# Kernel tuning notes

Hardware: AMD Instinct MI355X
Metric: run time of the kernel (lower is better)

The kernel has to match this reference:

```python
import jax, jax.numpy as jnp
import numpy as np

N = 2048
H = 128
W = 128
NEAR = 0.1


def _quat_to_rotmat(q):
    # q: [N,4] (w,x,y,z), normalized -> [N,3,3]
    q = q / jnp.clip(jnp.linalg.norm(q, axis=1, keepdims=True), 1e-8)
    w, x, y, z = q[:, 0], q[:, 1], q[:, 2], q[:, 3]
    xx, yy, zz = x * x, y * y, z * z
    xy, xz, yz = x * y, x * z, y * z
    wx, wy, wz = w * x, w * y, w * z
    r0 = jnp.stack([1 - 2 * (yy + zz), 2 * (xy - wz), 2 * (xz + wy)], axis=1)
    r1 = jnp.stack([2 * (xy + wz), 1 - 2 * (xx + zz), 2 * (yz - wx)], axis=1)
    r2 = jnp.stack([2 * (xz - wy), 2 * (yz + wx), 1 - 2 * (xx + yy)], axis=1)
    return jnp.stack([r0, r1, r2], axis=1)


def _covariance_matrices(log_scales, rotations):
    # R diag(s^2) R^T + 1e-6 I, per Gaussian
    s2 = jnp.exp(2.0 * log_scales)  # scales**2
    R = _quat_to_rotmat(rotations)  # [N,3,3]
    cov = jnp.einsum('nij,nj,nkj->nik', R, s2, R)
    return cov + 1e-6 * jnp.eye(3, dtype=cov.dtype)


def _render(means, cov3d, colors, opacities, intrinsics, camera_to_world, height, width):
    dt = means.dtype
    Rcw = camera_to_world[:3, :3]
    tcw = camera_to_world[:3, 3]
    Rwc = Rcw.T
    twc = -Rwc @ tcw
    p = means @ Rwc.T + twc  # [N,3] camera-space
    x, y, z = p[:, 0], p[:, 1], p[:, 2]
    valid = (z > NEAR).astype(dt)
    zc = jnp.maximum(z, NEAR)
    fx, fy = intrinsics[0, 0], intrinsics[1, 1]
    cx, cy = intrinsics[0, 2], intrinsics[1, 2]
    u = fx * x / zc + cx
    v = fy * y / zc + cy
    # EWA projection Jacobian [N,2,3]
    zeros = jnp.zeros_like(zc)
    J0 = jnp.stack([fx / zc, zeros, -fx * x / (zc * zc)], axis=1)
    J1 = jnp.stack([zeros, fy / zc, -fy * y / (zc * zc)], axis=1)
    J = jnp.stack([J0, J1], axis=1)
    cov_cam = jnp.einsum('ij,njk,lk->nil', Rwc, cov3d, Rwc)  # [N,3,3]
    cov2d = jnp.einsum('nij,njk,nlk->nil', J, cov_cam, J) + 0.3 * jnp.eye(2, dtype=dt)
    a, b, c = cov2d[:, 0, 0], cov2d[:, 0, 1], cov2d[:, 1, 1]
    det = jnp.maximum(a * c - b * b, 1e-12)
    cA, cB, cC = c / det, -b / det, a / det  # conic (inverse 2D covariance)
    # front-to-back depth order; invalid Gaussians pushed to the back
    order = jnp.argsort(jnp.where(valid > 0, zc, jnp.inf))
    u, v = u[order], v[order]
    cA, cB, cC = cA[order], cB[order], cC[order]
    op = (opacities * valid)[order]
    cols = colors[order]
    xs = jnp.arange(width, dtype=dt)
    ys = jnp.arange(height, dtype=dt)
    dx = xs[None, None, :] - u[:, None, None]  # [N,1,W] -> broadcasts
    dy = ys[None, :, None] - v[:, None, None]  # [N,H,1]
    power = (-0.5 * (cA[:, None, None] * dx * dx + cC[:, None, None] * dy * dy)
             - cB[:, None, None] * dx * dy)  # [N,H,W]
    power = jnp.minimum(power, 0.0)
    alpha = jnp.clip(op[:, None, None] * jnp.exp(power), 0.0, 0.99)
    Tcum = jnp.cumprod(1.0 - alpha, axis=0)
    Texcl = jnp.concatenate([jnp.ones_like(Tcum[:1]), Tcum[:-1]], axis=0)
    weight = alpha * Texcl  # [N,H,W]
    img = jnp.einsum('nhw,nc->hwc', weight, cols)  # [H,W,3]
    return img


def setup_inputs():
    key = jax.random.key(0)
    k = jax.random.split(key, 6)
    xy = jax.random.uniform(k[0], (N, 2), minval=-2.0, maxval=2.0)
    z = jax.random.uniform(k[1], (N, 1), minval=3.0, maxval=9.0)
    means = jnp.concatenate([xy, z], axis=1)
    log_scales = jnp.log(jax.random.uniform(k[2], (N, 3), minval=0.02, maxval=0.2))
    rotations = jax.random.normal(k[3], (N, 4))
    colors = jax.random.uniform(k[4], (N, 3))
    opacities = jax.random.normal(k[5], (N,))
    intrinsics = jnp.array([[150.0, 0.0, W / 2], [0.0, 150.0, H / 2], [0.0, 0.0, 1.0]], dtype=jnp.float32)
    camera_to_world = jnp.eye(4, dtype=jnp.float32)
    return {"means": means, "log_scales": log_scales, "rotations": rotations,
            "colors": colors, "opacities": opacities, "intrinsics": intrinsics,
            "camera_to_world": camera_to_world, "height": H, "width": W}


def reference(means, log_scales, rotations, colors, opacities, intrinsics, camera_to_world, height, width):
    cov3d = _covariance_matrices(log_scales, rotations)
    return _render(means, cov3d, jnp.clip(colors, 0.0, 1.0), jax.nn.sigmoid(opacities),
                   intrinsics, camera_to_world, height, width)
```

## Files before the change

### kernel.cpp

```cpp
#include <hip/hip_runtime.h>
#include <hip/hip_bf16.h>

#define NMAX 2048
#define HH 128
#define WW 128
#define NSEG 8
#define SEG 256
#define NEARP 0.1f

static __device__ __forceinline__ float ldin(const void* p, int i, bool is32) {
    return is32 ? ((const float*)p)[i]
                : __bfloat162float(((const __hip_bfloat16*)p)[i]);
}
static __device__ __forceinline__ bool detect32(const void* intr) {
    return ((const float*)intr)[0] > 1.0f;
}
static __device__ __forceinline__ void stout(void* out, int i, float v, bool is32) {
    if (is32) ((float*)out)[i] = v;
    else      ((__hip_bfloat16*)out)[i] = __float2bfloat16(v);
}


__global__ __launch_bounds__(256) void gs_preprocess(
    const void* __restrict__ means,
    const void* __restrict__ log_scales,
    const void* __restrict__ rots,
    const void* __restrict__ colors,
    const void* __restrict__ opac,
    const void* __restrict__ intr,
    const void* __restrict__ c2w,
    int n,
    unsigned long long* __restrict__ keys,
    float* __restrict__ params)
{
    int i = blockIdx.x * blockDim.x + threadIdx.x;
    if (i >= NMAX) return;
    bool is32 = detect32(intr);
    if (i >= n) {
        keys[i] = (((unsigned long long)0x7f800000u) << 32) | (unsigned int)i;
        return;
    }

    float Rwc[3][3], twc[3];
    {
        float Rcw[3][3], tcw[3];
        for (int r = 0; r < 3; ++r) {
            for (int c = 0; c < 3; ++c) Rcw[r][c] = ldin(c2w, r * 4 + c, is32);
            tcw[r] = ldin(c2w, r * 4 + 3, is32);
        }
        for (int r = 0; r < 3; ++r)
            for (int c = 0; c < 3; ++c) Rwc[r][c] = Rcw[c][r];
        for (int r = 0; r < 3; ++r)
            twc[r] = -(Rwc[r][0] * tcw[0] + Rwc[r][1] * tcw[1] + Rwc[r][2] * tcw[2]);
    }
    float fx = ldin(intr, 0, is32), fy = ldin(intr, 4, is32);
    float cx = ldin(intr, 2, is32), cy = ldin(intr, 5, is32);

    float mx = ldin(means, 3 * i, is32), my = ldin(means, 3 * i + 1, is32),
          mz = ldin(means, 3 * i + 2, is32);
    float px = Rwc[0][0] * mx + Rwc[0][1] * my + Rwc[0][2] * mz + twc[0];
    float py = Rwc[1][0] * mx + Rwc[1][1] * my + Rwc[1][2] * mz + twc[1];
    float pz = Rwc[2][0] * mx + Rwc[2][1] * my + Rwc[2][2] * mz + twc[2];
    bool valid = pz > NEARP;
    float zc = fmaxf(pz, NEARP);
    float izc = 1.0f / zc;
    float u = fx * px * izc + cx;
    float v = fy * py * izc + cy;

    float qw = ldin(rots, 4 * i, is32), qx = ldin(rots, 4 * i + 1, is32),
          qy = ldin(rots, 4 * i + 2, is32), qz = ldin(rots, 4 * i + 3, is32);
    float nrm = sqrtf(qw * qw + qx * qx + qy * qy + qz * qz);
    float inv = 1.0f / fmaxf(nrm, 1e-8f);
    qw *= inv; qx *= inv; qy *= inv; qz *= inv;
    float xx = qx * qx, yy = qy * qy, zz = qz * qz;
    float xy = qx * qy, xz = qx * qz, yz = qy * qz;
    float wx = qw * qx, wy = qw * qy, wz = qw * qz;
    float R[3][3] = {
        {1.f - 2.f * (yy + zz), 2.f * (xy - wz),       2.f * (xz + wy)},
        {2.f * (xy + wz),       1.f - 2.f * (xx + zz), 2.f * (yz - wx)},
        {2.f * (xz - wy),       2.f * (yz + wx),       1.f - 2.f * (xx + yy)}
    };
    float s2[3];
    for (int k = 0; k < 3; ++k) s2[k] = __expf(2.0f * ldin(log_scales, 3 * i + k, is32));

    float M[3][3];
    for (int r = 0; r < 3; ++r)
        for (int c = 0; c < 3; ++c)
            M[r][c] = R[r][0] * s2[0] * R[c][0] + R[r][1] * s2[1] * R[c][1]
                    + R[r][2] * s2[2] * R[c][2];
    M[0][0] += 1e-6f; M[1][1] += 1e-6f; M[2][2] += 1e-6f;

    float TM[3][3];
    for (int r = 0; r < 3; ++r)
        for (int c = 0; c < 3; ++c)
            TM[r][c] = Rwc[r][0] * M[0][c] + Rwc[r][1] * M[1][c] + Rwc[r][2] * M[2][c];
    float CC[3][3];
    for (int r = 0; r < 3; ++r)
        for (int c = 0; c < 3; ++c)
            CC[r][c] = TM[r][0] * Rwc[c][0] + TM[r][1] * Rwc[c][1] + TM[r][2] * Rwc[c][2];

    float J0[3] = {fx * izc, 0.0f, -fx * px * izc * izc};
    float J1[3] = {0.0f, fy * izc, -fy * py * izc * izc};
    float t0[3], t1[3];
    for (int c = 0; c < 3; ++c) {
        t0[c] = J0[0] * CC[0][c] + J0[1] * CC[1][c] + J0[2] * CC[2][c];
        t1[c] = J1[0] * CC[0][c] + J1[1] * CC[1][c] + J1[2] * CC[2][c];
    }
    float a  = t0[0] * J0[0] + t0[1] * J0[1] + t0[2] * J0[2] + 0.3f;
    float bq = t0[0] * J1[0] + t0[1] * J1[1] + t0[2] * J1[2];
    float cq = t1[0] * J1[0] + t1[1] * J1[1] + t1[2] * J1[2] + 0.3f;
    float det = fmaxf(a * cq - bq * bq, 1e-12f);
    float idet = 1.0f / det;
    float cA = cq * idet, cB = -bq * idet, cCc = a * idet;

    float o  = ldin(opac, i, is32);
    float op = valid ? (1.0f / (1.0f + __expf(-o))) : 0.0f;
    float cr = fminf(fmaxf(ldin(colors, 3 * i, is32), 0.f), 1.f);
    float cg = fminf(fmaxf(ldin(colors, 3 * i + 1, is32), 0.f), 1.f);
    float cb = fminf(fmaxf(ldin(colors, 3 * i + 2, is32), 0.f), 1.f);

    float zkey = valid ? zc : __builtin_inff();
    keys[i] = (((unsigned long long)__float_as_uint(zkey)) << 32) | (unsigned int)i;

    float* p = params + i * 12;
    p[0] = u;  p[1] = v;
    p[2] = -0.5f * cA;
    p[3] = -cB;
    p[4] = -0.5f * cCc;
    p[5] = op;
    p[6] = cr; p[7] = cg; p[8] = cb; p[9] = 0.f; p[10] = 0.f; p[11] = 0.f;
}

__global__ __launch_bounds__(256) void gs_rank_scatter(
    const unsigned long long* __restrict__ keys_in,
    const float* __restrict__ params_in,
    float* __restrict__ params_sorted,
    int n)
{
    __shared__ unsigned long long sk[NMAX];
    __shared__ int pr[32][9];
    __shared__ int rk[32];
    int t = threadIdx.x;
    #pragma unroll
    for (int e = 0; e < 8; ++e) sk[t + e * 256] = keys_in[t + e * 256];
    __syncthreads();

    int g0 = blockIdx.x * 32;
    int gi = t >> 3;
    int c  = t & 7;
    unsigned long long mykey = sk[g0 + gi];
    int cnt = 0;
    #pragma unroll 8
    for (int j = c; j < NMAX; j += 8)
        cnt += (sk[j] < mykey) ? 1 : 0;
    pr[gi][c] = cnt;
    __syncthreads();

    if (t < 32) {
        int r = 0;
        #pragma unroll
        for (int k = 0; k < 8; ++k) r += pr[t][k];
        rk[t] = r;
    }
    __syncthreads();

    if (t < 96) {
        int g = t / 3, q = t % 3;
        int src = g0 + g;
        float4 val;
        if (src < n) val = ((const float4*)params_in)[src * 3 + q];
        else         val = make_float4(0.f, 0.f, 0.f, 0.f);
        ((float4*)params_sorted)[rk[g] * 3 + q] = val;
    }
}

__global__ __launch_bounds__(256) void gs_render(
    const float* __restrict__ params_sorted,
    float4* __restrict__ segbuf)
{
    __shared__ float sp[SEG * 12];
    int seg = blockIdx.y;
    int t = threadIdx.x;

    const float4* src = (const float4*)(params_sorted + seg * SEG * 12);
    float4* dst = (float4*)sp;
    #pragma unroll
    for (int k = t; k < SEG * 3; k += 256) dst[k] = src[k];
    __syncthreads();

    int pid0 = (blockIdx.x * 256 + t) * 2;
    float px0 = (float)(pid0 & (WW - 1));
    float px1 = px0 + 1.0f;
    float py  = (float)(pid0 >> 7);

    float T0 = 1.f, r0 = 0.f, g0 = 0.f, b0 = 0.f;
    float T1 = 1.f, r1 = 0.f, g1 = 0.f, b1 = 0.f;
    #pragma unroll 4
    for (int i = 0; i < SEG; ++i) {
        const float* gp = sp + i * 12;
        float4 A = *(const float4*)(gp);
        float4 B = *(const float4*)(gp + 4);
        float4 C = *(const float4*)(gp + 8);
        float dy    = py - A.y;
        float nbdy  = A.w * dy;
        float ncdy2 = (B.x * dy) * dy;

        float dx0 = px0 - A.x;
        float p0 = fmaf(fmaf(A.z, dx0, nbdy), dx0, ncdy2);
        p0 = fminf(p0, 0.0f);
        float al0 = fminf(B.y * __expf(p0), 0.99f);
        float w0 = al0 * T0;
        r0 = fmaf(w0, B.z, r0);
        g0 = fmaf(w0, B.w, g0);
        b0 = fmaf(w0, C.x, b0);
        T0 *= (1.0f - al0);

        float dx1 = px1 - A.x;
        float p1 = fmaf(fmaf(A.z, dx1, nbdy), dx1, ncdy2);
        p1 = fminf(p1, 0.0f);
        float al1 = fminf(B.y * __expf(p1), 0.99f);
        float w1 = al1 * T1;
        r1 = fmaf(w1, B.z, r1);
        g1 = fmaf(w1, B.w, g1);
        b1 = fmaf(w1, C.x, b1);
        T1 *= (1.0f - al1);
    }
    segbuf[seg * (HH * WW) + pid0]     = make_float4(r0, g0, b0, T0);
    segbuf[seg * (HH * WW) + pid0 + 1] = make_float4(r1, g1, b1, T1);
}

__global__ __launch_bounds__(256) void gs_combine(
    const float4* __restrict__ segbuf,
    void* __restrict__ out,
    const void* __restrict__ intr)
{
    int pid = blockIdx.x * 256 + threadIdx.x;
    if (pid >= HH * WW) return;
    bool is32 = detect32(intr);
    float r = 0.f, g = 0.f, b = 0.f, T = 1.0f;
    #pragma unroll
    for (int s = 0; s < NSEG; ++s) {
        float4 vv = segbuf[s * (HH * WW) + pid];
        r = fmaf(T, vv.x, r);
        g = fmaf(T, vv.y, g);
        b = fmaf(T, vv.z, b);
        T *= vv.w;
    }
    stout(out, pid * 3 + 0, r, is32);
    stout(out, pid * 3 + 1, g, is32);
    stout(out, pid * 3 + 2, b, is32);
}

__global__ __launch_bounds__(256) void gs_render_all(
    const float* __restrict__ params_sorted,
    void* __restrict__ out,
    const void* __restrict__ intr)
{
    __shared__ float sp[SEG * 12];
    int t = threadIdx.x;
    int pid = blockIdx.x * 256 + t;
    bool is32 = detect32(intr);
    float pxf = (float)(pid & (WW - 1));
    float pyf = (float)(pid >> 7);

    float T = 1.f, r = 0.f, g = 0.f, b = 0.f;
    for (int seg = 0; seg < NSEG; ++seg) {
        __syncthreads();
        const float4* src = (const float4*)(params_sorted + seg * SEG * 12);
        float4* dst = (float4*)sp;
        #pragma unroll
        for (int k = t; k < SEG * 3; k += 256) dst[k] = src[k];
        __syncthreads();
        for (int i = 0; i < SEG; ++i) {
            const float* gp = sp + i * 12;
            float dx = pxf - gp[0];
            float dy = pyf - gp[1];
            float pwr = fmaf(fmaf(gp[2], dx, gp[3] * dy), dx, (gp[4] * dy) * dy);
            pwr = fminf(pwr, 0.0f);
            float alpha = fminf(gp[5] * __expf(pwr), 0.99f);
            float wgt = alpha * T;
            r = fmaf(wgt, gp[6], r);
            g = fmaf(wgt, gp[7], g);
            b = fmaf(wgt, gp[8], b);
            T *= (1.0f - alpha);
        }
    }
    stout(out, pid * 3 + 0, r, is32);
    stout(out, pid * 3 + 1, g, is32);
    stout(out, pid * 3 + 2, b, is32);
}

extern "C" void kernel_launch(void* const* d_in, const int* in_sizes, int n_in,
                              void* d_out, int out_size, void* d_ws, size_t ws_size,
                              hipStream_t stream)
{
    const void* means      = d_in[0];
    const void* log_scales = d_in[1];
    const void* rotations  = d_in[2];
    const void* colors     = d_in[3];
    const void* opacities  = d_in[4];
    const void* intrinsics = d_in[5];
    const void* cam2world  = d_in[6];

    int n = in_sizes[4];
    if (n > NMAX) n = NMAX;

    size_t off_keys   = 0;
    size_t off_params = NMAX * 8;
    size_t off_sorted = off_params + NMAX * 48;
    size_t off_seg    = off_sorted + NMAX * 48;
    size_t need_seg   = off_seg + (size_t)NSEG * HH * WW * 16;

    unsigned long long* keys = (unsigned long long*)((char*)d_ws + off_keys);
    float* params  = (float*)((char*)d_ws + off_params);
    float* sortedp = (float*)((char*)d_ws + off_sorted);
    float4* segbuf = (float4*)((char*)d_ws + off_seg);

    gs_preprocess<<<NMAX / 256, 256, 0, stream>>>(
        means, log_scales, rotations, colors, opacities, intrinsics, cam2world,
        n, keys, params);
    gs_rank_scatter<<<NMAX / 32, 256, 0, stream>>>(keys, params, sortedp, n);

    if (ws_size >= need_seg) {
        dim3 rg(HH * WW / 512, NSEG);
        gs_render<<<rg, 256, 0, stream>>>(sortedp, segbuf);
        gs_combine<<<HH * WW / 256, 256, 0, stream>>>(segbuf, d_out, intrinsics);
    } else {
        gs_render_all<<<HH * WW / 256, 256, 0, stream>>>(sortedp, d_out, intrinsics);
    }
}
```

Before: 100.4 us.

## Cull Gaussians per 32x16 screen tile before compositing each depth segment

The render kernel now assigns each block a 32x16 pixel tile and has it test every Gaussian in its depth segment against a per-Gaussian analytic bound on the tile. The bound uses the quadratic-form maxima along x and y plus log-opacity, all precomputed in preprocessing. Surviving Gaussians are compacted into shared memory with ballot/popcount, and the compositing loop runs only over that count. Segments change to 16 of 128 Gaussians. This skips exp/blend work for Gaussians that cannot reach the tile, at the cost of a ballot/compaction step and extra combine work from more segments; contributions below exp(-18) are dropped.

New measurement: 88.48 us, median of 2. 1.13x faster.

```diff
diff --git a/kernel.cpp b/kernel.cpp
--- a/kernel.cpp
+++ b/kernel.cpp
@@ -4,9 +4,10 @@
 #define NMAX 2048
 #define HH 128
 #define WW 128
-#define NSEG 8
-#define SEG 256
+#define NSEG 16
+#define SEG 128
 #define NEARP 0.1f
+#define CULL_LOG_EPS -18.0f
 
 static __device__ __forceinline__ float ldin(const void* p, int i, bool is32) {
     return is32 ? ((const float*)p)[i]
@@ -122,13 +123,19 @@
     float zkey = valid ? zc : __builtin_inff();
     keys[i] = (((unsigned long long)__float_as_uint(zkey)) << 32) | (unsigned int)i;
 
+    float na  = -0.5f * cA;
+    float nb  = -cB;
+    float ncc = -0.5f * cCc;
+    float qyb = ncc - nb * nb / (4.0f * na);
+    float qxb = na  - nb * nb / (4.0f * ncc);
+    float lnop = __logf(op);
+
     float* p = params + i * 12;
     p[0] = u;  p[1] = v;
-    p[2] = -0.5f * cA;
-    p[3] = -cB;
-    p[4] = -0.5f * cCc;
+    p[2] = na;  p[3] = nb;  p[4] = ncc;
     p[5] = op;
-    p[6] = cr; p[7] = cg; p[8] = cb; p[9] = 0.f; p[10] = 0.f; p[11] = 0.f;
+    p[6] = cr; p[7] = cg; p[8] = cb;
+    p[9] = qyb; p[10] = lnop; p[11] = qxb;
 }
 
 __global__ __launch_bounds__(256) void gs_rank_scatter(
@@ -179,24 +186,48 @@
     float4* __restrict__ segbuf)
 {
     __shared__ float sp[SEG * 12];
+    __shared__ int swcnt[2];
     int seg = blockIdx.y;
     int t = threadIdx.x;
-
-    const float4* src = (const float4*)(params_sorted + seg * SEG * 12);
-    float4* dst = (float4*)sp;
-    #pragma unroll
-    for (int k = t; k < SEG * 3; k += 256) dst[k] = src[k];
-    __syncthreads();
-
-    int pid0 = (blockIdx.x * 256 + t) * 2;
-    float px0 = (float)(pid0 & (WW - 1));
+    int x0 = (blockIdx.x & 3) * 32;
+    int y0 = (blockIdx.x >> 2) * 16;
+
+    float4 a4, b4, c4;
+    bool keep = false;
+    if (t < SEG) {
+        const float4* src = (const float4*)(params_sorted + (seg * SEG + t) * 12);
+        a4 = src[0];
+        b4 = src[1];
+        c4 = src[2];
+        float dxm = fmaxf(fmaxf((float)x0 - a4.x, a4.x - (float)(x0 + 31)), 0.0f);
+        float dym = fmaxf(fmaxf((float)y0 - a4.y, a4.y - (float)(y0 + 15)), 0.0f);
+        float bound = fminf(c4.y * dym * dym, c4.w * dxm * dxm) + c4.z;
+        keep = (bound > CULL_LOG_EPS) && (b4.y > 0.0f);
+    }
+    unsigned long long ball = __ballot(keep);
+    int lane = t & 63, wid = t >> 6;
+    if (lane == 0 && wid < 2) swcnt[wid] = (int)__popcll(ball);
+    __syncthreads();
+    int M = swcnt[0] + swcnt[1];
+    if (keep) {
+        int rank = (wid ? swcnt[0] : 0)
+                 + (int)__popcll(ball & ((1ull << lane) - 1ull));
+        float4* d = (float4*)(sp + rank * 12);
+        d[0] = a4; d[1] = b4; d[2] = c4;
+    }
+    __syncthreads();
+
+    int col = x0 + ((t & 15) << 1);
+    int row = y0 + (t >> 4);
+    float px0 = (float)col;
     float px1 = px0 + 1.0f;
-    float py  = (float)(pid0 >> 7);
+    float py  = (float)row;
+    int pid0 = row * WW + col;
 
     float T0 = 1.f, r0 = 0.f, g0 = 0.f, b0 = 0.f;
     float T1 = 1.f, r1 = 0.f, g1 = 0.f, b1 = 0.f;
-    #pragma unroll 4
-    for (int i = 0; i < SEG; ++i) {
+    #pragma unroll 2
+    for (int i = 0; i < M; ++i) {
         const float* gp = sp + i * 12;
         float4 A = *(const float4*)(gp);
         float4 B = *(const float4*)(gp + 4);
@@ -322,7 +353,7 @@
     gs_rank_scatter<<<NMAX / 32, 256, 0, stream>>>(keys, params, sortedp, n);
 
     if (ws_size >= need_seg) {
-        dim3 rg(HH * WW / 512, NSEG);
+        dim3 rg(32, NSEG);
         gs_render<<<rg, 256, 0, stream>>>(sortedp, segbuf);
         gs_combine<<<HH * WW / 256, 256, 0, stream>>>(segbuf, d_out, intrinsics);
     } else {
```

## Replace segmented full-frame render with tiled render and per-tile Gaussian culling

Applied to the files above, without the earlier changes.

Preprocessing now stores per-Gaussian bounds on the quadratic exponent and the log opacity. The render kernel processes 16x16 pixel tiles, one block per tile, with sorted Gaussians streamed in chunks of 256. Each chunk is compacted with a wave ballot into a list of Gaussians that can contribute above a small threshold to the tile. This removes most exp and blend work per pixel, along with the segment buffer and the combine kernel. The cost is only 64 blocks of parallelism, extra barriers per chunk, and a negligible approximation from dropping tiny contributions.

Result: slower. 123.2 us (+22.7%).

```diff
diff --git a/kernel.cpp b/kernel.cpp
--- a/kernel.cpp
+++ b/kernel.cpp
@@ -4,9 +4,9 @@
 #define NMAX 2048
 #define HH 128
 #define WW 128
-#define NSEG 8
-#define SEG 256
 #define NEARP 0.1f
+#define CULL_LOG_EPS -18.0f
+#define CHUNK 256
 
 static __device__ __forceinline__ float ldin(const void* p, int i, bool is32) {
     return is32 ? ((const float*)p)[i]
@@ -122,13 +122,19 @@
     float zkey = valid ? zc : __builtin_inff();
     keys[i] = (((unsigned long long)__float_as_uint(zkey)) << 32) | (unsigned int)i;
 
+    float na  = -0.5f * cA;
+    float nb  = -cB;
+    float ncc = -0.5f * cCc;
+    float qyb = ncc - nb * nb / (4.0f * na);
+    float qxb = na  - nb * nb / (4.0f * ncc);
+    float lnop = __logf(op);
+
     float* p = params + i * 12;
     p[0] = u;  p[1] = v;
-    p[2] = -0.5f * cA;
-    p[3] = -cB;
-    p[4] = -0.5f * cCc;
+    p[2] = na;  p[3] = nb;  p[4] = ncc;
     p[5] = op;
-    p[6] = cr; p[7] = cg; p[8] = cb; p[9] = 0.f; p[10] = 0.f; p[11] = 0.f;
+    p[6] = cr; p[7] = cg; p[8] = cb;
+    p[9] = qyb; p[10] = lnop; p[11] = qxb;
 }
 
 __global__ __launch_bounds__(256) void gs_rank_scatter(
@@ -174,120 +180,91 @@
     }
 }
 
-__global__ __launch_bounds__(256) void gs_render(
-    const float* __restrict__ params_sorted,
-    float4* __restrict__ segbuf)
-{
-    __shared__ float sp[SEG * 12];
-    int seg = blockIdx.y;
-    int t = threadIdx.x;
-
-    const float4* src = (const float4*)(params_sorted + seg * SEG * 12);
-    float4* dst = (float4*)sp;
-    #pragma unroll
-    for (int k = t; k < SEG * 3; k += 256) dst[k] = src[k];
-    __syncthreads();
-
-    int pid0 = (blockIdx.x * 256 + t) * 2;
-    float px0 = (float)(pid0 & (WW - 1));
-    float px1 = px0 + 1.0f;
-    float py  = (float)(pid0 >> 7);
-
-    float T0 = 1.f, r0 = 0.f, g0 = 0.f, b0 = 0.f;
-    float T1 = 1.f, r1 = 0.f, g1 = 0.f, b1 = 0.f;
-    #pragma unroll 4
-    for (int i = 0; i < SEG; ++i) {
-        const float* gp = sp + i * 12;
-        float4 A = *(const float4*)(gp);
-        float4 B = *(const float4*)(gp + 4);
-        float4 C = *(const float4*)(gp + 8);
-        float dy    = py - A.y;
-        float nbdy  = A.w * dy;
-        float ncdy2 = (B.x * dy) * dy;
-
-        float dx0 = px0 - A.x;
-        float p0 = fmaf(fmaf(A.z, dx0, nbdy), dx0, ncdy2);
-        p0 = fminf(p0, 0.0f);
-        float al0 = fminf(B.y * __expf(p0), 0.99f);
-        float w0 = al0 * T0;
-        r0 = fmaf(w0, B.z, r0);
-        g0 = fmaf(w0, B.w, g0);
-        b0 = fmaf(w0, C.x, b0);
-        T0 *= (1.0f - al0);
-
-        float dx1 = px1 - A.x;
-        float p1 = fmaf(fmaf(A.z, dx1, nbdy), dx1, ncdy2);
-        p1 = fminf(p1, 0.0f);
-        float al1 = fminf(B.y * __expf(p1), 0.99f);
-        float w1 = al1 * T1;
-        r1 = fmaf(w1, B.z, r1);
-        g1 = fmaf(w1, B.w, g1);
-        b1 = fmaf(w1, C.x, b1);
-        T1 *= (1.0f - al1);
-    }
-    segbuf[seg * (HH * WW) + pid0]     = make_float4(r0, g0, b0, T0);
-    segbuf[seg * (HH * WW) + pid0 + 1] = make_float4(r1, g1, b1, T1);
-}
-
-__global__ __launch_bounds__(256) void gs_combine(
-    const float4* __restrict__ segbuf,
-    void* __restrict__ out,
-    const void* __restrict__ intr)
-{
-    int pid = blockIdx.x * 256 + threadIdx.x;
-    if (pid >= HH * WW) return;
-    bool is32 = detect32(intr);
-    float r = 0.f, g = 0.f, b = 0.f, T = 1.0f;
-    #pragma unroll
-    for (int s = 0; s < NSEG; ++s) {
-        float4 vv = segbuf[s * (HH * WW) + pid];
-        r = fmaf(T, vv.x, r);
-        g = fmaf(T, vv.y, g);
-        b = fmaf(T, vv.z, b);
-        T *= vv.w;
-    }
-    stout(out, pid * 3 + 0, r, is32);
-    stout(out, pid * 3 + 1, g, is32);
-    stout(out, pid * 3 + 2, b, is32);
-}
-
-__global__ __launch_bounds__(256) void gs_render_all(
+__global__ __launch_bounds__(256) void gs_render_tiles(
     const float* __restrict__ params_sorted,
     void* __restrict__ out,
     const void* __restrict__ intr)
 {
-    __shared__ float sp[SEG * 12];
+    __shared__ __align__(16) float schunk[CHUNK * 12];
+    __shared__ unsigned short sidx[CHUNK];
+    __shared__ int wcnt[4];
+
     int t = threadIdx.x;
-    int pid = blockIdx.x * 256 + t;
+    int lane = t & 63, wid = t >> 6;
     bool is32 = detect32(intr);
-    float pxf = (float)(pid & (WW - 1));
-    float pyf = (float)(pid >> 7);
-
-    float T = 1.f, r = 0.f, g = 0.f, b = 0.f;
-    for (int seg = 0; seg < NSEG; ++seg) {
-        __syncthreads();
-        const float4* src = (const float4*)(params_sorted + seg * SEG * 12);
-        float4* dst = (float4*)sp;
+    int bx = blockIdx.x & 7, by = blockIdx.x >> 3;
+    float tx0 = (float)(bx * 16), tx1 = tx0 + 15.0f;
+    float ty0 = (float)(by * 16), ty1 = ty0 + 15.0f;
+    float pxf = tx0 + (float)(t & 15);
+    float pyf = ty0 + (float)(t >> 4);
+
+    const float4* src = (const float4*)params_sorted;
+    float4 r0 = src[t * 3 + 0];
+    float4 r1 = src[t * 3 + 1];
+    float4 r2 = src[t * 3 + 2];
+
+    float T = 1.f, cr = 0.f, cg = 0.f, cb = 0.f;
+
+    for (int c = 0; c < NMAX / CHUNK; ++c) {
+        float4* dst = (float4*)(schunk + t * 12);
+        dst[0] = r0; dst[1] = r1; dst[2] = r2;
+        __syncthreads();
+
+        float u    = schunk[t * 12 + 0];
+        float v    = schunk[t * 12 + 1];
+        float op   = schunk[t * 12 + 5];
+        float qyb  = schunk[t * 12 + 9];
+        float lnop = schunk[t * 12 + 10];
+        float qxb  = schunk[t * 12 + 11];
+        float dxm = fmaxf(fmaxf(tx0 - u, u - tx1), 0.0f);
+        float dym = fmaxf(fmaxf(ty0 - v, v - ty1), 0.0f);
+        bool keep = (fminf(qyb * dym * dym, qxb * dxm * dxm) + lnop > CULL_LOG_EPS)
+                  && (op > 0.0f);
+        unsigned long long ball = __ballot(keep);
+        if (lane == 0) wcnt[wid] = (int)__popcll(ball);
+        __syncthreads();
+        int base = 0, Msc = 0;
         #pragma unroll
-        for (int k = t; k < SEG * 3; k += 256) dst[k] = src[k];
-        __syncthreads();
-        for (int i = 0; i < SEG; ++i) {
-            const float* gp = sp + i * 12;
-            float dx = pxf - gp[0];
-            float dy = pyf - gp[1];
-            float pwr = fmaf(fmaf(gp[2], dx, gp[3] * dy), dx, (gp[4] * dy) * dy);
+        for (int w = 0; w < 4; ++w) {
+            if (w < wid) base += wcnt[w];
+            Msc += wcnt[w];
+        }
+        if (keep)
+            sidx[base + (int)__popcll(ball & ((1ull << lane) - 1ull))] =
+                (unsigned short)t;
+        __syncthreads();
+
+        if (c + 1 < NMAX / CHUNK) {
+            int nt = (c + 1) * CHUNK + t;
+            r0 = src[nt * 3 + 0];
+            r1 = src[nt * 3 + 1];
+            r2 = src[nt * 3 + 2];
+        }
+
+        #pragma unroll 2
+        for (int i = 0; i < Msc; ++i) {
+            const float* gp = schunk + (int)sidx[i] * 12;
+            float4 A = *(const float4*)(gp);
+            float4 B = *(const float4*)(gp + 4);
+            float4 C = *(const float4*)(gp + 8);
+            float dy = pyf - A.y;
+            float dx = pxf - A.x;
+            float pwr = fmaf(fmaf(A.z, dx, A.w * dy), dx, (B.x * dy) * dy);
             pwr = fminf(pwr, 0.0f);
-            float alpha = fminf(gp[5] * __expf(pwr), 0.99f);
-            float wgt = alpha * T;
-            r = fmaf(wgt, gp[6], r);
-            g = fmaf(wgt, gp[7], g);
-            b = fmaf(wgt, gp[8], b);
-            T *= (1.0f - alpha);
-        }
-    }
-    stout(out, pid * 3 + 0, r, is32);
-    stout(out, pid * 3 + 1, g, is32);
-    stout(out, pid * 3 + 2, b, is32);
+            float al = fminf(B.y * __expf(pwr), 0.99f);
+            float w = al * T;
+            cr = fmaf(w, B.z, cr);
+            cg = fmaf(w, B.w, cg);
+            cb = fmaf(w, C.x, cb);
+            T *= (1.0f - al);
+        }
+        __syncthreads();
+    }
+
+    int pid = (by * 16 + (t >> 4)) * WW + bx * 16 + (t & 15);
+    stout(out, pid * 3 + 0, cr, is32);
+    stout(out, pid * 3 + 1, cg, is32);
+    stout(out, pid * 3 + 2, cb, is32);
 }
 
 extern "C" void kernel_launch(void* const* d_in, const int* in_sizes, int n_in,
@@ -305,27 +282,13 @@
     int n = in_sizes[4];
     if (n > NMAX) n = NMAX;
 
-    size_t off_keys   = 0;
-    size_t off_params = NMAX * 8;
-    size_t off_sorted = off_params + NMAX * 48;
-    size_t off_seg    = off_sorted + NMAX * 48;
-    size_t need_seg   = off_seg + (size_t)NSEG * HH * WW * 16;
-
-    unsigned long long* keys = (unsigned long long*)((char*)d_ws + off_keys);
-    float* params  = (float*)((char*)d_ws + off_params);
-    float* sortedp = (float*)((char*)d_ws + off_sorted);
-    float4* segbuf = (float4*)((char*)d_ws + off_seg);
+    unsigned long long* keys = (unsigned long long*)d_ws;
+    float* params  = (float*)((char*)d_ws + NMAX * 8);
+    float* sortedp = (float*)((char*)d_ws + NMAX * 8 + NMAX * 48);
 
     gs_preprocess<<<NMAX / 256, 256, 0, stream>>>(
         means, log_scales, rotations, colors, opacities, intrinsics, cam2world,
         n, keys, params);
     gs_rank_scatter<<<NMAX / 32, 256, 0, stream>>>(keys, params, sortedp, n);
-
-    if (ws_size >= need_seg) {
-        dim3 rg(HH * WW / 512, NSEG);
-        gs_render<<<rg, 256, 0, stream>>>(sortedp, segbuf);
-        gs_combine<<<HH * WW / 256, 256, 0, stream>>>(segbuf, d_out, intrinsics);
-    } else {
-        gs_render_all<<<HH * WW / 256, 256, 0, stream>>>(sortedp, d_out, intrinsics);
-    }
-}
+    gs_render_tiles<<<64, 256, 0, stream>>>(sortedp, d_out, intrinsics);
+}
```
